# Kernel tuning notes

Measured on AMD Instinct MI355X. Metric: run time of the kernel, lower is better.

## Reference

```python
import jax, jax.numpy as jnp
import numpy as np
import math

DIM = 768
NUM_HEADS = 16
PERHEAD = DIM // NUM_HEADS  # 48
B, T = 4, 2048


def setup_inputs() -> dict:
    key = jax.random.key(0)
    k_x, k_wi, k_bi, k_wo, k_bo = jax.random.split(key, 5)
    s_in = 1.0 / math.sqrt(DIM)
    return {
        "x": jax.random.normal(k_x, (B, T, DIM), dtype=jnp.float32),
        # linear_in: y = x @ w_in + b_in, w_in: (DIM, 3*DIM)
        "w_in": jax.random.uniform(k_wi, (DIM, 3 * DIM), jnp.float32, -s_in, s_in),
        "b_in": jax.random.uniform(k_bi, (3 * DIM,), jnp.float32, -s_in, s_in),
        "w_out": jax.random.uniform(k_wo, (DIM, DIM), jnp.float32, -s_in, s_in),
        "b_out": jax.random.uniform(k_bo, (DIM,), jnp.float32, -s_in, s_in),
    }


def reference(x, w_in, b_in, w_out, b_out):
    bs, tok, _ = x.shape
    qkv = x @ w_in + b_in                                   # (B, T, 3*DIM)
    # Faithful to torch: reshape to (B, T, H, 3*ph), move heads, chunk last dim.
    qkv = qkv.reshape(bs, tok, NUM_HEADS, 3 * PERHEAD)
    qkv = jnp.transpose(qkv, (0, 2, 1, 3))                  # (B, H, T, 3*ph)
    q, k, v = jnp.split(qkv, 3, axis=-1)                    # each (B, H, T, ph)
    scale = 1.0 / math.sqrt(PERHEAD)
    scores = jnp.einsum("bhqd,bhkd->bhqk", q, k) * scale    # (B, H, T, T)
    attn = jax.nn.softmax(scores, axis=-1)
    # dropout p=0.0 (eval) -> identity
    out = jnp.einsum("bhqk,bhkd->bhqd", attn, v)            # (B, H, T, ph)
    out = jnp.transpose(out, (0, 2, 1, 3)).reshape(bs, tok, DIM)
    return out @ w_out + b_out
```

## Files before the change

kernel.cpp:

```cpp
#include <hip/hip_runtime.h>
#include <hip/hip_bf16.h>
#include <math.h>

typedef __attribute__((ext_vector_type(8))) short short8;
typedef __attribute__((ext_vector_type(4))) float floatx4;
typedef __hip_bfloat16 bf16;

#define DIM 768
#define NHEADS 16
#define PH 48
#define VROWS 49
#define BATCH 4
#define SEQ 2048
#define MTOK (BATCH*SEQ)
#define NQKV (3*DIM)
#define NQK (2*DIM)
#define LOG2E 1.44269504088896f
#define CFAC (0.14433756729740643f * LOG2E)

#define NB_CAST   6144
#define NB_TWIN   1728
#define NB_TWOUT  576
#define NB_MISC   140

__device__ __forceinline__ void cp16(void* dst, const void* src) {
    *(float4*)dst = *(const float4*)src;
}
__device__ __forceinline__ unsigned short f2us(float v) {
    bf16 b = __float2bfloat16(v);
    return *(unsigned short*)&b;
}
__device__ __forceinline__ float us2f(unsigned short u) {
    bf16 b = *(bf16*)&u;
    return __bfloat162float(b);
}
__device__ __forceinline__ void gload_lds16(const bf16* g, bf16* l) {
    __builtin_amdgcn_global_load_lds(
        (const __attribute__((address_space(1))) unsigned int*)g,
        (__attribute__((address_space(3))) unsigned int*)l, 16, 0, 0);
}
__device__ __forceinline__ bool sniff_f32(const unsigned short* __restrict__ x) {
    float v = us2f(x[threadIdx.x & 63]);
    int bad = !(fabsf(v) < 64.0f);
    return __any(bad) != 0;
}

__global__ __launch_bounds__(256) void prep_all(
    const void* __restrict__ x, const void* __restrict__ w_in,
    const void* __restrict__ w_out, const void* __restrict__ bin,
    const void* __restrict__ bout,
    bf16* __restrict__ xb, bf16* __restrict__ winT, bf16* __restrict__ woutT,
    float* __restrict__ bi, float* __restrict__ bo, bf16* __restrict__ Vt)
{
    __shared__ bf16 tile[32][33];
    const int bid = blockIdx.x, tid = threadIdx.x;
    const bool f32 = sniff_f32((const unsigned short*)x);

    if (bid < NB_CAST) {
        int i = bid * 256 + tid;
        if (f32) {
            float4 v = ((const float4*)x)[i];
            ushort4 o;
            o.x = f2us(v.x); o.y = f2us(v.y); o.z = f2us(v.z); o.w = f2us(v.w);
            ((ushort4*)xb)[i] = o;
        } else {
            ((ushort4*)xb)[i] = ((const ushort4*)x)[i];
        }
    } else if (bid < NB_CAST + NB_TWIN + NB_TWOUT) {
        const void* in; bf16* out; int R, C, tt;
        if (bid < NB_CAST + NB_TWIN) {
            in = w_in; out = winT; R = DIM; C = NQKV; tt = bid - NB_CAST;
        } else {
            in = w_out; out = woutT; R = DIM; C = DIM; tt = bid - NB_CAST - NB_TWIN;
        }
        int ctiles = C / 32;
        int c0 = (tt % ctiles) * 32, r0 = (tt / ctiles) * 32;
        int tx = tid & 31, ty = tid >> 5;
#pragma unroll
        for (int j = 0; j < 4; j++) {
            size_t idx = (size_t)(r0 + ty + 8*j) * C + c0 + tx;
            float v = f32 ? ((const float*)in)[idx]
                          : us2f(((const unsigned short*)in)[idx]);
            tile[ty + 8*j][tx] = __float2bfloat16(v);
        }
        __syncthreads();
#pragma unroll
        for (int j = 0; j < 4; j++)
            out[(size_t)(c0 + ty + 8*j) * R + r0 + tx] = tile[tx][ty + 8*j];
    } else {
        int t = (bid - (NB_CAST + NB_TWIN + NB_TWOUT)) * 256 + tid;
        if (t < NQKV) {
            bi[t] = f32 ? ((const float*)bin)[t] : us2f(((const unsigned short*)bin)[t]);
        } else if (t < NQKV + DIM) {
            int j = t - NQKV;
            bo[j] = f32 ? ((const float*)bout)[j] : us2f(((const unsigned short*)bout)[j]);
        } else {
            int k = t - (NQKV + DIM);
            int bh = k >> 9, pos = (k & 511) * 4;
            bf16* dst = Vt + ((size_t)bh * VROWS + 48) * SEQ + pos;
            ushort4 ones;
            ones.x = ones.y = ones.z = ones.w = f2us(1.0f);
            *(ushort4*)dst = ones;
        }
    }
}

template<int N, int MODE, int TM, int BK>
__global__ __launch_bounds__(256, (BK == 32 ? 4 : 1)) void gemm_bias(
    const bf16* __restrict__ A, const bf16* __restrict__ BT,
    const float* __restrict__ bias, void* __restrict__ C0, bf16* __restrict__ Vt,
    const unsigned short* __restrict__ xraw)
{
    constexpr int K = 768;
    constexpr int KSUB = BK / 32;
    constexpr int NSTEP = K / BK;
    constexpr int MI = TM / 32;
    constexpr int TS = TM * 32;
    constexpr int BS = 128 * 32;
    constexpr int BUFE = KSUB * (TS + BS);
    __shared__ __align__(16) bf16 smem[2 * BUFE];
    const bool out_f32 = (MODE == 2) && sniff_f32(xraw);
    const int tid = threadIdx.x;
    const int id = blockIdx.x;
    constexpr int NMB = MTOK / TM;
    const int m0 = (id % NMB) * TM, n0 = (id / NMB) * 128;
    const int w = tid >> 6, lane = tid & 63, lq = lane >> 4, ln = lane & 15;
    const int wr = w & 1, wc = w >> 1;

    const int ssw = ((lane >> 2) ^ (lane >> 4)) & 3;
    const int cm = (lane & 3) ^ ssw;
    const int rlB0 = w * 32 + (lane >> 2), rlB1 = rlB0 + 16;
    const int rlA  = (TM == 128) ? rlB0 : (w * 16 + (lane >> 2));
    const bf16* gA0 = A + (size_t)(m0 + rlA) * K + cm * 8;
    const bf16* gA1 = A + (size_t)(m0 + rlA + ((TM == 128) ? 16 : 0)) * K + cm * 8;
    const bf16* gB0 = BT + (size_t)(n0 + rlB0) * K + cm * 8;
    const bf16* gB1 = BT + (size_t)(n0 + rlB1) * K + cm * 8;
    bf16* lA0 = smem + ((TM == 128) ? (w * 32) * 32 : (w * 16) * 32);
    bf16* lA1 = smem + (w * 32 + 16) * 32;
    bf16* lB0 = smem + KSUB * TS + (w * 32) * 32;
    bf16* lB1 = smem + KSUB * TS + (w * 32 + 16) * 32;

    const int rsw = (ln ^ (ln >> 2)) & 3;
    const int rchunk = (lq ^ rsw) * 8;

    floatx4 zero4 = {0.f, 0.f, 0.f, 0.f};
    floatx4 acc[MI][4];
#pragma unroll
    for (int mi = 0; mi < MI; mi++)
#pragma unroll
        for (int nj = 0; nj < 4; nj++) acc[mi][nj] = zero4;

#define STAGE_TILE(BO) do {                                                  \
    _Pragma("unroll")                                                        \
    for (int ks = 0; ks < KSUB; ks++) {                                      \
        gload_lds16(gA0 + 32 * ks, lA0 + (BO) + ks * TS);                    \
        if constexpr (TM == 128)                                             \
            gload_lds16(gA1 + 32 * ks, lA1 + (BO) + ks * TS);                \
        gload_lds16(gB0 + 32 * ks, lB0 + (BO) + ks * BS);                    \
        gload_lds16(gB1 + 32 * ks, lB1 + (BO) + ks * BS);                    \
    }                                                                        \
    gA0 += BK; gA1 += BK; gB0 += BK; gB1 += BK;                              \
} while (0)

    STAGE_TILE(0);
    __syncthreads();

    for (int step = 0; step < NSTEP; step++) {
        if (step < NSTEP - 1)
            STAGE_TILE(((step + 1) & 1) * BUFE);
        const int co = (step & 1) * BUFE;
#pragma unroll
        for (int kk = 0; kk < KSUB; kk++) {
            const bf16* Asub = smem + co + kk * TS;
            const bf16* Bsub = smem + co + KSUB * TS + kk * BS;
            short8 a[MI], b[4];
#pragma unroll
            for (int mi = 0; mi < MI; mi++)
                a[mi] = *(const short8*)&Asub[(wr * (TM/2) + 16 * mi + ln) * 32 + rchunk];
#pragma unroll
            for (int nj = 0; nj < 4; nj++)
                b[nj] = *(const short8*)&Bsub[(wc * 64 + 16 * nj + ln) * 32 + rchunk];
#pragma unroll
            for (int mi = 0; mi < MI; mi++)
#pragma unroll
                for (int nj = 0; nj < 4; nj++)
                    acc[mi][nj] = __builtin_amdgcn_mfma_f32_16x16x32_bf16(
                        a[mi], b[nj], acc[mi][nj], 0, 0, 0);
        }
        __syncthreads();
    }
#undef STAGE_TILE

    bf16 (*VLs)[136] = (bf16(*)[136])smem;

#pragma unroll
    for (int nj = 0; nj < 4; nj++) {
        int n = n0 + wc * 64 + 16 * nj + ln;
        float bv = bias[n];
        if (MODE == 2) {
#pragma unroll
            for (int mi = 0; mi < MI; mi++)
#pragma unroll
                for (int i = 0; i < 4; i++) {
                    size_t off = (size_t)(m0 + wr * (TM/2) + 16 * mi + 4 * lq + i) * N + n;
                    float val = acc[mi][nj][i] + bv;
                    if (out_f32) ((float*)C0)[off] = val;
                    else         ((bf16*)C0)[off] = __float2bfloat16(val);
                }
        } else {
            int h = n / 144, r = n - 144 * h;
            if (r < 96) {
                float sc = (r < 48) ? CFAC : 1.0f;
#pragma unroll
                for (int mi = 0; mi < MI; mi++)
#pragma unroll
                    for (int i = 0; i < 4; i++) {
                        size_t off = (size_t)(m0 + wr * (TM/2) + 16 * mi + 4 * lq + i) * NQK
                                     + h * 96 + r;
                        ((bf16*)C0)[off] = __float2bfloat16((acc[mi][nj][i] + bv) * sc);
                    }
            } else {
                int d = r - 96;
#pragma unroll
                for (int mi = 0; mi < MI; mi++)
#pragma unroll
                    for (int i = 0; i < 4; i++)
                        VLs[d][wr * 64 + 32 * (mi >> 1) + 8 * lq + 4 * (mi & 1) + i] =
                            __float2bfloat16(acc[mi][nj][i] + bv);
            }
        }
    }

    if (MODE == 1) {
        __syncthreads();
        const int bidx = m0 >> 11, tok0 = m0 & 2047;
#pragma unroll
        for (int s = 0; s < 3; s++) {
            int idx = tid + 256 * s;
            int d = idx >> 4, ch = idx & 15;
            int h = (n0 + 31 - d) / 144;
            int n = 144 * h + 96 + d;
            if (n >= n0 && n < n0 + 128) {
                bf16* dst = Vt + ((size_t)(bidx * NHEADS + h) * VROWS + d) * SEQ
                            + tok0 + ch * 8;
                *(float4*)dst = *(const float4*)&VLs[d][ch * 8];
            }
        }
    }
}

__global__ __launch_bounds__(256, 2) void attn_fused(
    const bf16* __restrict__ QK, const bf16* __restrict__ Vt, bf16* __restrict__ O)
{
    __shared__ bf16 Ks[4][64][72];
    __shared__ bf16 VsT[4][64][72];

    const int tid = threadIdx.x;
    const int id = blockIdx.x;
    const int g = id & 63, qt = id >> 6;
    const int h = g & 15, b = g >> 4;
    const int w = tid >> 6, lane = tid & 63, lq = lane >> 4, ln = lane & 15;
    const size_t rowbase = (size_t)b * SEQ;
    const int q0 = qt * 256;
    const int hoff = h * 96;
    const bf16* Vth = Vt + (size_t)(b * NHEADS + h) * VROWS * SEQ;

    const bf16 bzero = __float2bfloat16(0.f);
    for (int idx = tid; idx < 4096; idx += 256) {
        int rg = idx >> 10, r = (idx >> 4) & 63, c = idx & 15;
        Ks[rg][r][48 + c] = bzero;
    }

    short8 qa0[4], qa1[4];
    short8 zero8 = {0, 0, 0, 0, 0, 0, 0, 0};
#pragma unroll
    for (int f = 0; f < 4; f++) {
        const bf16* qrow = QK + (rowbase + q0 + 64*f + 16*w + ln) * NQK + hoff;
        qa0[f] = *(const short8*)(qrow + lq * 8);
        qa1[f] = (lq < 2) ? *(const short8*)(qrow + 32 + lq * 8) : zero8;
    }

    const int kr0a = tid / 6, kc0a = tid % 6;
    const int kr1a = (tid + 256) / 6, kc1a = (tid + 256) % 6;
    const char* kg0 = (const char*)(QK + (rowbase + kr0a) * NQK + hoff + 48) + kc0a * 16;
    const char* kg1 = (const char*)(QK + (rowbase + kr1a) * NQK + hoff + 48) + kc1a * 16;
    bf16* kd0 = &Ks[0][kr0a][kc0a * 8];
    bf16* kd1 = &Ks[0][kr1a & 63][kc1a * 8];
    const bool kact = (tid < 128);
    const int vr0 = tid >> 3, vc0 = tid & 7;
    const char* vg0 = (const char*)(Vth + (size_t)vr0 * SEQ) + vc0 * 16;
    const char* vg1 = (const char*)(Vth + (size_t)(32 + vr0) * SEQ) + vc0 * 16;
    bf16* vd0 = &VsT[0][vr0][vc0 * 8];
    bf16* vd1 = &VsT[0][32 + vr0][vc0 * 8];
    const bool vact = (tid < 136);
    const ptrdiff_t KOFF = (ptrdiff_t)64 * NQK * 2;
    const ptrdiff_t KADV = (ptrdiff_t)128 * NQK * 2;
    const ptrdiff_t VOFF = 128, VADV = 256;
    const int SOFF = 64 * 72;

    floatx4 zero4 = {0.f, 0.f, 0.f, 0.f};
    floatx4 o[4][4];
#pragma unroll
    for (int f = 0; f < 4; f++)
#pragma unroll
        for (int nt = 0; nt < 4; nt++) o[f][nt] = zero4;

    float4 rka0, rka1, rva0, rva1;
    float4 rkb0, rkb1, rvb0, rvb1;

#define PREFETCH() do {                                                      \
    rka0 = *(const float4*)kg0;                                              \
    rkb0 = *(const float4*)(kg0 + KOFF);                                     \
    rva0 = *(const float4*)vg0;                                              \
    rvb0 = *(const float4*)(vg0 + VOFF);                                     \
    if (kact) { rka1 = *(const float4*)kg1;                                  \
                rkb1 = *(const float4*)(kg1 + KOFF); }                       \
    if (vact) { rva1 = *(const float4*)vg1;                                  \
                rvb1 = *(const float4*)(vg1 + VOFF); }                       \
    kg0 += KADV; kg1 += KADV; vg0 += VADV; vg1 += VADV;                       \
} while (0)

#define STAGE(RG) do {                                                       \
    *(float4*)(kd0 + (RG) * SOFF)       = rka0;                              \
    *(float4*)(kd0 + ((RG) + 1) * SOFF) = rkb0;                              \
    if (kact) { *(float4*)(kd1 + (RG) * SOFF)       = rka1;                  \
                *(float4*)(kd1 + ((RG) + 1) * SOFF) = rkb1; }                \
    *(float4*)(vd0 + (RG) * SOFF)       = rva0;                              \
    *(float4*)(vd0 + ((RG) + 1) * SOFF) = rvb0;                              \
    if (vact) { *(float4*)(vd1 + (RG) * SOFF)       = rva1;                  \
                *(float4*)(vd1 + ((RG) + 1) * SOFF) = rvb1; }                \
} while (0)

#define SUBTILE(RG) do {                                                     \
    const bf16 (*Kc)[72] = Ks[RG];                                           \
    const bf16 (*Vc)[72] = VsT[RG];                                          \
    short8 kb0[4], kb1[4];                                                   \
    _Pragma("unroll")                                                        \
    for (int t = 0; t < 4; t++) {                                            \
        kb0[t] = *(const short8*)&Kc[16*t + ln][lq * 8];                     \
        kb1[t] = *(const short8*)&Kc[16*t + ln][lq * 8 + 32];                \
    }                                                                        \
    short8 pa[4][2];                                                         \
    _Pragma("unroll")                                                        \
    for (int f = 0; f < 4; f++) {                                            \
        floatx4 s[4];                                                        \
        _Pragma("unroll")                                                    \
        for (int t = 0; t < 4; t++) {                                        \
            s[t] = zero4;                                                    \
            s[t] = __builtin_amdgcn_mfma_f32_16x16x32_bf16(kb0[t], qa0[f], s[t], 0, 0, 0); \
            s[t] = __builtin_amdgcn_mfma_f32_16x16x32_bf16(kb1[t], qa1[f], s[t], 0, 0, 0); \
        }                                                                    \
        _Pragma("unroll")                                                    \
        for (int ks = 0; ks < 2; ks++) {                                     \
            union { short8 v; __hip_bfloat162 h2[4]; } u;                    \
            float2 p;                                                        \
            p.x = __builtin_amdgcn_exp2f(s[2*ks][0]);                        \
            p.y = __builtin_amdgcn_exp2f(s[2*ks][1]);                        \
            u.h2[0] = __float22bfloat162_rn(p);                              \
            p.x = __builtin_amdgcn_exp2f(s[2*ks][2]);                        \
            p.y = __builtin_amdgcn_exp2f(s[2*ks][3]);                        \
            u.h2[1] = __float22bfloat162_rn(p);                              \
            p.x = __builtin_amdgcn_exp2f(s[2*ks+1][0]);                      \
            p.y = __builtin_amdgcn_exp2f(s[2*ks+1][1]);                      \
            u.h2[2] = __float22bfloat162_rn(p);                              \
            p.x = __builtin_amdgcn_exp2f(s[2*ks+1][2]);                      \
            p.y = __builtin_amdgcn_exp2f(s[2*ks+1][3]);                      \
            u.h2[3] = __float22bfloat162_rn(p);                              \
            pa[f][ks] = u.v;                                                 \
        }                                                                    \
    }                                                                        \
    _Pragma("unroll")                                                        \
    for (int nt = 0; nt < 4; nt++) {                                         \
        short8 vb0 = *(const short8*)&Vc[16*nt + ln][lq * 8];                \
        short8 vb1 = *(const short8*)&Vc[16*nt + ln][lq * 8 + 32];           \
        _Pragma("unroll")                                                    \
        for (int f = 0; f < 4; f++) {                                        \
            o[f][nt] = __builtin_amdgcn_mfma_f32_16x16x32_bf16(pa[f][0], vb0, o[f][nt], 0, 0, 0); \
            o[f][nt] = __builtin_amdgcn_mfma_f32_16x16x32_bf16(pa[f][1], vb1, o[f][nt], 0, 0, 0); \
        }                                                                    \
    }                                                                        \
} while (0)

    PREFETCH();
    STAGE(0);
    PREFETCH();
    __syncthreads();

    for (int ko = 0; ko < 16; ko++) {
        const int cur = ko & 1;
        if (ko < 15) {
            STAGE((cur ^ 1) * 2);
            if (ko < 14) PREFETCH();
        }
        __builtin_amdgcn_s_setprio(1);
        SUBTILE(cur * 2);
        SUBTILE(cur * 2 + 1);
        __builtin_amdgcn_s_setprio(0);
        __syncthreads();
    }

#undef SUBTILE
#undef STAGE
#undef PREFETCH

#pragma unroll
    for (int f = 0; f < 4; f++)
#pragma unroll
        for (int i = 0; i < 4; i++) {
            float l = __shfl(o[f][3][i], (lane >> 4) << 4);
            float inv = 1.0f / l;
            int row = q0 + 64*f + 16*w + 4*lq + i;
#pragma unroll
            for (int nt = 0; nt < 3; nt++)
                O[(rowbase + row) * DIM + h * PH + 16*nt + ln] =
                    __float2bfloat16(o[f][nt][i] * inv);
        }
}

extern "C" void kernel_launch(void* const* d_in, const int* in_sizes, int n_in,
                              void* d_out, int out_size, void* d_ws, size_t ws_size,
                              hipStream_t stream) {
    const void* x     = d_in[0];
    const void* w_in  = d_in[1];
    const void* b_in  = d_in[2];
    const void* w_out = d_in[3];
    const void* b_out = d_in[4];

    bf16* qk    = (bf16*)d_ws;
    bf16* Vt    = qk    + (size_t)MTOK * NQK;
    bf16* xb    = Vt    + (size_t)BATCH * NHEADS * VROWS * SEQ;
    bf16* attn  = xb;
    bf16* winT  = xb    + (size_t)MTOK * DIM;
    bf16* woutT = winT  + (size_t)NQKV * DIM;
    float* bi   = (float*)(woutT + (size_t)DIM * DIM);
    float* bo   = bi + NQKV;

    prep_all<<<NB_CAST + NB_TWIN + NB_TWOUT + NB_MISC, 256, 0, stream>>>(
        x, w_in, w_out, b_in, b_out, xb, winT, woutT, bi, bo, Vt);

    gemm_bias<NQKV, 1, 128, 32><<<64 * (NQKV/128), 256, 0, stream>>>(
        xb, winT, bi, qk, Vt, (const unsigned short*)x);
    attn_fused<<<64 * (SEQ/256), 256, 0, stream>>>(qk, Vt, attn);
    gemm_bias<DIM, 2, 64, 64><<<128 * (DIM/128), 256, 0, stream>>>(
        attn, woutT, bo, d_out, nullptr, (const unsigned short*)x);
}
```

Before: 205.7 us.

## Prefetch two K-tiles ahead in GEMM with explicit vmcnt waits, BK=64 everywhere

Restructures the GEMM main loop so two K-tiles are in flight. The next tile is issued right after each compute step, and a partial s_waitcnt vmcnt waits only for the older tile instead of draining all loads at __syncthreads. It also fixes BK at 64 for both GEMMs, which doubles shared memory for the QKV GEMM and drops the occupancy hint of 4 blocks per SM. This aims to hide global-to-LDS latency better, but it can lower occupancy for the large QKV GEMM, and the vmcnt counts must match the number of loads issued per stage.

New measurement: 206.2 us. No clear change (+0.3%).

```diff
diff --git a/kernel.cpp b/kernel.cpp
--- a/kernel.cpp
+++ b/kernel.cpp
@@ -105,13 +105,14 @@
     }
 }
 
-template<int N, int MODE, int TM, int BK>
-__global__ __launch_bounds__(256, (BK == 32 ? 4 : 1)) void gemm_bias(
+template<int N, int MODE, int TM>
+__global__ __launch_bounds__(256) void gemm_bias(
     const bf16* __restrict__ A, const bf16* __restrict__ BT,
     const float* __restrict__ bias, void* __restrict__ C0, bf16* __restrict__ Vt,
     const unsigned short* __restrict__ xraw)
 {
     constexpr int K = 768;
+    constexpr int BK = 64;
     constexpr int KSUB = BK / 32;
     constexpr int NSTEP = K / BK;
     constexpr int MI = TM / 32;
@@ -162,12 +163,18 @@
     gA0 += BK; gA1 += BK; gB0 += BK; gB1 += BK;                              \
 } while (0)
 
+#define WAIT_PREV() do {                                                     \
+    if constexpr (TM == 128) asm volatile("s_waitcnt vmcnt(8)" ::: "memory");\
+    else                     asm volatile("s_waitcnt vmcnt(6)" ::: "memory");\
+    __builtin_amdgcn_sched_barrier(0);                                       \
+} while (0)
+
     STAGE_TILE(0);
-    __syncthreads();
+    STAGE_TILE(BUFE);
+    WAIT_PREV();
+    __builtin_amdgcn_s_barrier();
 
     for (int step = 0; step < NSTEP; step++) {
-        if (step < NSTEP - 1)
-            STAGE_TILE(((step + 1) & 1) * BUFE);
         const int co = (step & 1) * BUFE;
 #pragma unroll
         for (int kk = 0; kk < KSUB; kk++) {
@@ -187,8 +194,17 @@
                     acc[mi][nj] = __builtin_amdgcn_mfma_f32_16x16x32_bf16(
                         a[mi], b[nj], acc[mi][nj], 0, 0, 0);
         }
-        __syncthreads();
-    }
+        __builtin_amdgcn_s_barrier();
+        if (step + 2 < NSTEP) {
+            STAGE_TILE(co);
+            WAIT_PREV();
+        } else {
+            asm volatile("s_waitcnt vmcnt(0)" ::: "memory");
+            __builtin_amdgcn_sched_barrier(0);
+        }
+        __builtin_amdgcn_s_barrier();
+    }
+#undef WAIT_PREV
 #undef STAGE_TILE
 
     bf16 (*VLs)[136] = (bf16(*)[136])smem;
@@ -438,9 +454,9 @@
     prep_all<<<NB_CAST + NB_TWIN + NB_TWOUT + NB_MISC, 256, 0, stream>>>(
         x, w_in, w_out, b_in, b_out, xb, winT, woutT, bi, bo, Vt);
 
-    gemm_bias<NQKV, 1, 128, 32><<<64 * (NQKV/128), 256, 0, stream>>>(
+    gemm_bias<NQKV, 1, 128><<<64 * (NQKV/128), 256, 0, stream>>>(
         xb, winT, bi, qk, Vt, (const unsigned short*)x);
     attn_fused<<<64 * (SEQ/256), 256, 0, stream>>>(qk, Vt, attn);
-    gemm_bias<DIM, 2, 64, 64><<<128 * (DIM/128), 256, 0, stream>>>(
+    gemm_bias<DIM, 2, 64><<<128 * (DIM/128), 256, 0, stream>>>(
         attn, woutT, bo, d_out, nullptr, (const unsigned short*)x);
 }
```
